# Performance work log

Measured on AMD Instinct MI355X. Metric: run time of the kernel, lower is better.

Reference implementation:

```python
import jax, jax.numpy as jnp
import numpy as np

N_NODES = 50000
N_EDGES = 800000
NUM_GRAPHS = 500
BN_EPS = 1e-5


def setup_inputs() -> dict:
    key = jax.random.key(0)
    ks = jax.random.split(key, 8)
    x = jax.random.normal(ks[0], (N_NODES, 33), dtype=jnp.float32)
    edge_index = jax.random.randint(ks[1], (2, N_EDGES), 0, N_NODES, dtype=jnp.int64)
    batch = jnp.sort(jax.random.randint(ks[2], (N_NODES,), 0, NUM_GRAPHS, dtype=jnp.int64))
    # Xavier-ish scaled weights
    W0 = jax.random.normal(ks[3], (33, 100), dtype=jnp.float32) * (2.0 / (33 + 100)) ** 0.5
    Wrest = jax.random.normal(ks[4], (3, 100, 100), dtype=jnp.float32) * (2.0 / 200) ** 0.5
    b = jnp.zeros((4, 100), dtype=jnp.float32)
    gamma = jnp.ones((4, 100), dtype=jnp.float32)
    beta = jnp.zeros((4, 100), dtype=jnp.float32)
    Wout = jax.random.normal(ks[5], (100, 200), dtype=jnp.float32) * (2.0 / 300) ** 0.5
    bout = jnp.zeros((200,), dtype=jnp.float32)
    return {"x": x, "edge_index": edge_index, "batch": batch, "W0": W0,
            "Wrest": Wrest, "b": b, "gamma": gamma, "beta": beta,
            "Wout": Wout, "bout": bout}


def reference(x, edge_index, batch, W0, Wrest, b, gamma, beta, Wout, bout):
    N = x.shape[0]
    # GCN normalization with self-loops (gcn_norm): shared across layers
    loops = jnp.arange(N, dtype=edge_index.dtype)
    src = jnp.concatenate([edge_index[0], loops])
    dst = jnp.concatenate([edge_index[1], loops])
    deg = jax.ops.segment_sum(jnp.ones_like(dst, dtype=x.dtype), dst, num_segments=N)
    dinv = jnp.where(deg > 0, jax.lax.rsqrt(deg), 0.0)
    norm = dinv[src] * dinv[dst]  # [E+N]

    Ws = [W0, Wrest[0], Wrest[1], Wrest[2]]
    h = x
    for layer in range(4):
        m = h @ Ws[layer]                                   # [N, out_c]
        agg = jax.ops.segment_sum(norm[:, None] * m[src], dst, num_segments=N)
        agg = agg + b[layer]
        # BatchNorm1d (batch statistics, biased variance)
        mean = agg.mean(axis=0)
        var = agg.var(axis=0)
        hbn = (agg - mean) * jax.lax.rsqrt(var + BN_EPS) * gamma[layer] + beta[layer]
        h = jax.nn.relu(hbn) if layer < 3 else hbn          # dropout is identity in eval

    g = jax.ops.segment_sum(h, batch, num_segments=NUM_GRAPHS)  # global_add_pool
    out = g @ Wout + bout
    return jnp.where(out > 0, out, 0.1 * out)  # LeakyReLU(0.1)
```

## Files before the change

### kernel.cpp

```cpp
#include <hip/hip_runtime.h>

#define NNODES 50000
#define NEDGES 800000
#define NGRAPH 500
#define CH 100
#define CIN0 33
#define BN_EPS 1e-5f
#define NSHARD 8
#define SHSTRIDE 1024
#define NBUK 196
#define BEPW 2048

#define SCAN_TPB 256
#define SCAN_IPT 4
#define SCAN_TILE (SCAN_TPB * SCAN_IPT)
#define SCAN_BLOCKS ((NNODES + SCAN_TILE - 1) / SCAN_TILE)

typedef __attribute__((ext_vector_type(8))) short short8;
typedef __attribute__((ext_vector_type(4))) float f32x4;

__device__ inline unsigned pack_bf16(float x, float y) {
    unsigned xb = __float_as_uint(x);
    unsigned yb = __float_as_uint(y);
    xb += 0x7FFF + ((xb >> 16) & 1);
    yb += 0x7FFF + ((yb >> 16) & 1);
    return (xb >> 16) | (yb & 0xFFFF0000u);
}
__device__ inline float unp_lo(unsigned v) { return __uint_as_float(v << 16); }
__device__ inline float unp_hi(unsigned v) { return __uint_as_float(v & 0xFFFF0000u); }

__global__ void k_prep(const float* __restrict__ x, unsigned* __restrict__ xb,
                       int* __restrict__ cnt, float* __restrict__ stats,
                       float* __restrict__ gbuf,
                       const float* __restrict__ Wrest, unsigned* __restrict__ whi,
                       unsigned* __restrict__ wlo,
                       const float* __restrict__ W0, unsigned* __restrict__ w0hi,
                       unsigned* __restrict__ w0lo,
                       unsigned* __restrict__ Z0, unsigned* __restrict__ Z1) {
    int i = blockIdx.x * blockDim.x + threadIdx.x;
    if (i < (NNODES + 1) * 17) {
        int r = i / 17, s = i - r * 17;
        if (r >= NNODES) xb[i] = 0u;
        else {
            float a = x[r * CIN0 + 2 * s];
            float b = (2 * s + 1 < CIN0) ? x[r * CIN0 + 2 * s + 1] : 0.f;
            xb[i] = pack_bf16(a, b);
        }
    }
    if (i < NNODES) { cnt[i] = 0; gbuf[i] = 0.f; }
    if (i < NSHARD * SHSTRIDE) stats[i] = 0.f;
    if (i < 3 * 112 * 64) {
        int l = i / 7168, rem = i % 7168;
        int c = rem >> 6, ku = rem & 63;
        int k0 = 2 * ku;
        float w0 = 0.f, w1 = 0.f;
        if (c < CH && k0 < CH) {
            w0 = Wrest[l * 10000 + k0 * CH + c];
            if (k0 + 1 < CH) w1 = Wrest[l * 10000 + (k0 + 1) * CH + c];
        }
        unsigned hh = pack_bf16(w0, w1);
        whi[i] = hh;
        wlo[i] = pack_bf16(w0 - unp_lo(hh), w1 - unp_hi(hh));
    }
    if (i < 112 * 32) {
        int c = i >> 5, ku = i & 31;
        int k0 = 2 * ku;
        float w0 = 0.f, w1 = 0.f;
        if (c < CH && k0 < CIN0) {
            w0 = W0[k0 * CH + c];
            if (k0 + 1 < CIN0) w1 = W0[(k0 + 1) * CH + c];
        }
        unsigned hh = pack_bf16(w0, w1);
        w0hi[i] = hh;
        w0lo[i] = pack_bf16(w0 - unp_lo(hh), w1 - unp_hi(hh));
    }
    if (i < 50) {
        Z0[(size_t)NNODES * 50 + i] = 0u;
        Z1[(size_t)NNODES * 50 + i] = 0u;
    }
}

__global__ void k_hist(const int* __restrict__ dst, int* __restrict__ cnt) {
    int e = blockIdx.x * blockDim.x + threadIdx.x;
    if (e < NEDGES) atomicAdd(&cnt[dst[e]], 1);
}

__global__ void k_scan1(const int* __restrict__ cnt, int* __restrict__ rowptr,
                        int* __restrict__ blkSums, float* __restrict__ dinv,
                        int* __restrict__ bcnt) {
    __shared__ int ts[SCAN_TPB];
    __shared__ int bsum[4];
    int tid = threadIdx.x;
    if (tid < 4) bsum[tid] = 0;
    int base = blockIdx.x * SCAN_TILE + tid * SCAN_IPT;
    int v[SCAN_IPT];
    int s = 0, cact = 0;
    #pragma unroll
    for (int j = 0; j < SCAN_IPT; ++j) {
        int i = base + j;
        int c = (i < NNODES) ? cnt[i] : 0;
        if (i < NNODES) dinv[i] = rsqrtf((float)(c + 1));
        v[j] = (c + 7) & ~7;
        s += v[j];
        cact += c;
    }
    ts[tid] = s;
    __syncthreads();
    atomicAdd(&bsum[(tid * SCAN_IPT) >> 8], cact);
    for (int off = 1; off < SCAN_TPB; off <<= 1) {
        int add = (tid >= off) ? ts[tid - off] : 0;
        __syncthreads();
        ts[tid] += add;
        __syncthreads();
    }
    int run = ts[tid] - s;
    #pragma unroll
    for (int j = 0; j < SCAN_IPT; ++j) {
        int i = base + j;
        if (i < NNODES) rowptr[i] = run;
        run += v[j];
    }
    if (tid == SCAN_TPB - 1) blkSums[blockIdx.x] = ts[tid];
    if (tid < 4) {
        int b = blockIdx.x * 4 + tid;
        if (b < NBUK) bcnt[b] = bsum[tid];
    }
}

__global__ void k_scan2b(const int* __restrict__ blkSums, int* __restrict__ blkOff,
                         int* __restrict__ rowptr, const int* __restrict__ bcnt,
                         int* __restrict__ bbase, int* __restrict__ gbkcur) {
    __shared__ int ts[256];
    int t = threadIdx.x;
    if (t == 0) {
        int run = 0;
        for (int i = 0; i < SCAN_BLOCKS; ++i) { blkOff[i] = run; run += blkSums[i]; }
        rowptr[NNODES] = run;
    }
    int v = (t < NBUK) ? bcnt[t] : 0;
    ts[t] = v;
    __syncthreads();
    for (int off = 1; off < 256; off <<= 1) {
        int a = (t >= off) ? ts[t - off] : 0;
        __syncthreads();
        ts[t] += a;
        __syncthreads();
    }
    int excl = ts[t] - v;
    if (t < NBUK) { bbase[t] = excl; gbkcur[t] = excl; }
    if (t == NBUK - 1) bbase[NBUK] = ts[t];
}

__global__ void k_scan3(int* __restrict__ rowptr, const int* __restrict__ blkOff) {
    int off = blkOff[blockIdx.x];
    int base = blockIdx.x * SCAN_TILE + threadIdx.x * SCAN_IPT;
    #pragma unroll
    for (int j = 0; j < SCAN_IPT; ++j) {
        int i = base + j;
        if (i < NNODES) rowptr[i] += off;
    }
}

__global__ __launch_bounds__(256) void k_bin(const int* __restrict__ src,
                                             const int* __restrict__ dst,
                                             const float* __restrict__ dinv,
                                             int* __restrict__ gbkcur,
                                             uint2* __restrict__ ebuf) {
    __shared__ int hist[256], ofs[256], lcnt[256], bbaseL[256];
    __shared__ int totS;
    __shared__ uint2 stage[BEPW];
    int tid = threadIdx.x;
    hist[tid] = 0; lcnt[tid] = 0;
    __syncthreads();
    int e0 = blockIdx.x * BEPW;
    unsigned sv[8]; int dv[8]; bool ok[8];
    #pragma unroll
    for (int j = 0; j < 8; ++j) {
        int e = e0 + j * 256 + tid;
        ok[j] = e < NEDGES;
        int s = ok[j] ? src[e] : 0;
        dv[j] = ok[j] ? dst[e] : 0;
        if (ok[j]) {
            unsigned db = __float_as_uint(dinv[s]);
            db += 0x7FFF + ((db >> 16) & 1);
            sv[j] = (unsigned)s | (db & 0xFFFF0000u);
            atomicAdd(&hist[dv[j] >> 8], 1);
        }
    }
    __syncthreads();
    int v = hist[tid];
    ofs[tid] = v;
    __syncthreads();
    for (int off = 1; off < 256; off <<= 1) {
        int a = (tid >= off) ? ofs[tid - off] : 0;
        __syncthreads();
        ofs[tid] += a;
        __syncthreads();
    }
    if (tid == 255) totS = ofs[255];
    int excl = ofs[tid] - v;
    __syncthreads();
    ofs[tid] = excl;
    if (tid < NBUK && v > 0) bbaseL[tid] = atomicAdd(&gbkcur[tid], v);
    __syncthreads();
    #pragma unroll
    for (int j = 0; j < 8; ++j) {
        if (ok[j]) {
            int b = dv[j] >> 8;
            int idx = atomicAdd(&lcnt[b], 1);
            stage[ofs[b] + idx] = make_uint2(sv[j], (unsigned)dv[j]);
        }
    }
    __syncthreads();
    int tot = totS;
    #pragma unroll
    for (int j = 0; j < 8; ++j) {
        int slot = j * 256 + tid;
        if (slot < tot) {
            uint2 p = stage[slot];
            int b = (int)(p.y >> 8);
            ebuf[bbaseL[b] + (slot - ofs[b])] = p;
        }
    }
}

__global__ __launch_bounds__(256) void k_place(const uint2* __restrict__ ebuf,
                                               const int* __restrict__ bbase,
                                               const int* __restrict__ rowptr,
                                               unsigned* __restrict__ ew) {
    __shared__ int lcur[256];
    int b = blockIdx.x, t = threadIdx.x;
    int lo = b * 256;
    int n = NNODES - lo; if (n > 256) n = 256;
    if (t < n) lcur[t] = rowptr[lo + t];
    __syncthreads();
    int e0 = bbase[b], e1 = bbase[b + 1];
    for (int e = e0 + t; e < e1; e += 256) {
        uint2 p = ebuf[e];
        int pos = atomicAdd(&lcur[p.y & 255], 1);
        ew[pos] = p.x;
    }
    __syncthreads();
    if (t < n) {
        int end = rowptr[lo + t + 1];
        for (int q = lcur[t]; q < end; ++q) ew[q] = NNODES;
    }
}

template<int CPACK, int RB, int KS, bool BN>
__global__ __launch_bounds__(512, 8) void k_fused(
    const unsigned* __restrict__ h, const unsigned* __restrict__ Whi,
    const unsigned* __restrict__ Wlo, const float* __restrict__ bias,
    const int* __restrict__ rowptr, const unsigned* __restrict__ ew,
    const float* __restrict__ dinv,
    const float* __restrict__ pgsum, const float* __restrict__ pgsq,
    const float* __restrict__ gamma, const float* __restrict__ beta,
    unsigned* __restrict__ Zout, float* __restrict__ gsum, float* __restrict__ gsq) {
    constexpr int RBY = KS * 64;
    __shared__ __align__(16) unsigned char aS[64 * RBY];
    __shared__ __align__(16) unsigned char wB[112 * 128];
    __shared__ float sSum[CH], sSq[CH];
    int tid = threadIdx.x;
    for (int i = tid; i < CH; i += 512) { sSum[i] = 0.f; sSq[i] = 0.f; }
    for (int idx = tid; idx < 112 * 8; idx += 512) {
        int c = idx >> 3, j = idx & 7;
        uint4 v = *(const uint4*)(Whi + c * (KS * 16) + j * 4);
        *(uint4*)(wB + ((unsigned)(c * 128 + j * 16) ^ ((c & 7) << 4))) = v;
    }
    int w = tid >> 6, lane = tid & 63;
    int row0 = blockIdx.x * 64;
    const char* __restrict__ hb = (const char*)h;
    bool act = lane < CPACK;
    unsigned l4 = (unsigned)(lane << 2);
    float scx = 0.f, shx = 0.f, scy = 0.f, shy = 0.f;
    if (BN && act) {
        float sx = 0.f, sy = 0.f, qx = 0.f, qy = 0.f;
        #pragma unroll
        for (int sh = 0; sh < NSHARD; ++sh) {
            float2 s2 = ((const float2*)(pgsum + sh * SHSTRIDE))[lane];
            float2 q2 = ((const float2*)(pgsq + sh * SHSTRIDE))[lane];
            sx += s2.x; sy += s2.y; qx += q2.x; qy += q2.y;
        }
        constexpr float invN = 1.f / NNODES;
        float2 g2 = ((const float2*)gamma)[lane];
        float2 b2 = ((const float2*)beta)[lane];
        float mx = sx * invN, my = sy * invN;
        float vx = qx * invN - mx * mx, vy = qy * invN - my * my;
        scx = g2.x * rsqrtf(vx + BN_EPS); shx = b2.x - mx * scx;
        scy = g2.y * rsqrtf(vy + BN_EPS); shy = b2.y - my * scy;
    }
    for (int ni = 0; ni < 8; ++ni) {
        int r = w * 8 + ni;
        int node = row0 + r;
        float ax = 0.f, ay = 0.f, di = 0.f;
        if (node < NNODES) {
            int p0 = __builtin_amdgcn_readfirstlane(rowptr[node]);
            int p1 = __builtin_amdgcn_readfirstlane(rowptr[node + 1]);
            di = dinv[node];
            if (act) {
                unsigned hv = h[(size_t)node * CPACK + lane];
                float fx = unp_lo(hv), fy = unp_hi(hv);
                if (BN) {
                    fx = fmaxf(fmaf(fx, scx, shx), 0.f);
                    fy = fmaxf(fmaf(fy, scy, shy), 0.f);
                }
                ax = di * fx; ay = di * fy;
            }
            const uint4* __restrict__ E4 = (const uint4*)(ew + p0);
            int n8 = (p1 - p0) >> 3;
            for (int q = 0; q < n8; ++q) {
                uint4 ea = E4[2 * q];
                uint4 eb = E4[2 * q + 1];
                unsigned ee[8] = {ea.x, ea.y, ea.z, ea.w, eb.x, eb.y, eb.z, eb.w};
                if (act) {
                    unsigned v[8];
                    #pragma unroll
                    for (int t = 0; t < 8; ++t)
                        v[t] = *(const unsigned*)(hb + (ee[t] & 0xFFFFu) * (unsigned)RB + l4);
                    #pragma unroll
                    for (int t = 0; t < 8; ++t) {
                        float vx = unp_lo(v[t]), vy = unp_hi(v[t]);
                        if (BN) {
                            vx = fmaxf(fmaf(vx, scx, shx), 0.f);
                            vy = fmaxf(fmaf(vy, scy, shy), 0.f);
                        }
                        float wgt = unp_hi(ee[t]);
                        ax = fmaf(wgt, vx, ax); ay = fmaf(wgt, vy, ay);
                    }
                }
            }
        }
        unsigned val = act ? pack_bf16(di * ax, di * ay) : 0u;
        if (lane < RBY / 4)
            *(unsigned*)(aS + ((unsigned)(r * RBY + lane * 4) ^ ((r & 7) << 4))) = val;
    }
    __syncthreads();
    int wm = w & 3, wh = w >> 2;
    int lr = lane & 15, lg = lane >> 4;
    f32x4 acc[4];
    #pragma unroll
    for (int nt = 0; nt < 4; ++nt) acc[nt] = (f32x4){0.f, 0.f, 0.f, 0.f};
    int ar = wm * 16 + lr;
    unsigned aswz = (unsigned)((ar & 7) << 4);
    #pragma unroll
    for (int ch = 0; ch < KS; ++ch) {
        if (ch) {
            __syncthreads();
            const unsigned* Wp = (ch >= KS / 2) ? Wlo : Whi;
            int p = (KS > 2) ? (ch & 1) : 0;
            for (int idx = tid; idx < 112 * 8; idx += 512) {
                int c = idx >> 3, j = idx & 7;
                uint4 v = *(const uint4*)(Wp + c * (KS * 16) + p * 32 + j * 4);
                *(uint4*)(wB + ((unsigned)(c * 128 + j * 16) ^ ((c & 7) << 4))) = v;
            }
            __syncthreads();
        }
        int p = (KS > 2) ? (ch & 1) : 0;
        #pragma unroll
        for (int ksl = 0; ksl < 2; ++ksl) {
            int ks = p * 2 + ksl;
            short8 af = *(const short8*)(aS + ((unsigned)(ar * RBY + ks * 64 + lg * 16) ^ aswz));
            #pragma unroll
            for (int nt = 0; nt < 4; ++nt) {
                if (wh && nt == 3) continue;
                int c = (wh * 4 + nt) * 16 + lr;
                short8 bb = *(const short8*)(wB + ((unsigned)(c * 128 + ksl * 64 + lg * 16) ^ ((c & 7) << 4)));
                acc[nt] = __builtin_amdgcn_mfma_f32_16x16x32_bf16(af, bb, acc[nt], 0, 0, 0);
            }
        }
    }
    #pragma unroll
    for (int nt = 0; nt < 4; ++nt) {
        if (wh && nt == 3) continue;
        int c = (wh * 4 + nt) * 16 + lr;
        bool cok = c < CH;
        float bcol = cok ? bias[c] : 0.f;
        float s = 0.f, q = 0.f;
        #pragma unroll
        for (int r = 0; r < 4; ++r) {
            int row = row0 + wm * 16 + lg * 4 + r;
            float z = acc[nt][r] + bcol;
            float zo = __shfl_xor(z, 1);
            if (cok && row < NNODES) {
                if ((lane & 1) == 0)
                    Zout[(size_t)row * 50 + (c >> 1)] = pack_bf16(z, zo);
                s += z; q += z * z;
            }
        }
        s += __shfl_xor(s, 16); s += __shfl_xor(s, 32);
        q += __shfl_xor(q, 16); q += __shfl_xor(q, 32);
        if (lane < 16 && cok) { atomicAdd(&sSum[c], s); atomicAdd(&sSq[c], q); }
    }
    __syncthreads();
    int sh = (blockIdx.x & (NSHARD - 1)) * SHSTRIDE;
    if (tid < CH) { atomicAdd(&gsum[sh + tid], sSum[tid]); atomicAdd(&gsq[sh + tid], sSq[tid]); }
}

__global__ void k_pool(const unsigned* __restrict__ Zl, const int* __restrict__ batch,
                       const float* __restrict__ gsum, const float* __restrict__ gsq,
                       const float* __restrict__ gamma, const float* __restrict__ beta,
                       float* __restrict__ g) {
    int gid = blockIdx.x;
    int part = blockIdx.y;
    int lo = 0, hi = NNODES;
    while (lo < hi) { int mid = (lo + hi) >> 1; if (batch[mid] < gid) lo = mid + 1; else hi = mid; }
    int start = lo;
    hi = NNODES;
    while (lo < hi) { int mid = (lo + hi) >> 1; if (batch[mid] < gid + 1) lo = mid + 1; else hi = mid; }
    int end = lo;
    int len = end - start;
    int cb = (len + 3) >> 2;
    int s = start + part * cb;
    int e = s + cb; if (e > end) e = end;
    if (s >= e) return;
    int t = threadIdx.x;
    if (t >= 50) return;
    float su = 0.f, sv = 0.f, qu = 0.f, qv = 0.f;
    #pragma unroll
    for (int sh = 0; sh < NSHARD; ++sh) {
        float2 s2 = ((const float2*)(gsum + sh * SHSTRIDE))[t];
        float2 q2 = ((const float2*)(gsq + sh * SHSTRIDE))[t];
        su += s2.x; sv += s2.y; qu += q2.x; qv += q2.y;
    }
    constexpr float invN = 1.f / NNODES;
    float2 g2 = ((const float2*)gamma)[t];
    float2 b2 = ((const float2*)beta)[t];
    float mx = su * invN, my = sv * invN;
    float vx = qu * invN - mx * mx, vy = qv * invN - my * my;
    float scx = g2.x * rsqrtf(vx + BN_EPS), shx = b2.x - mx * scx;
    float scy = g2.y * rsqrtf(vy + BN_EPS), shy = b2.y - my * scy;
    float sx = 0.f, sy = 0.f;
    for (int r = s; r < e; ++r) {
        unsigned v = Zl[(size_t)r * 50 + t];
        sx += unp_lo(v); sy += unp_hi(v);
    }
    float n = (float)(e - s);
    atomicAdd(&g[gid * CH + 2 * t], sx * scx + n * shx);
    atomicAdd(&g[gid * CH + 2 * t + 1], sy * scy + n * shy);
}

__global__ __launch_bounds__(256) void k_out(const float* __restrict__ g,
                                             const float* __restrict__ Wout,
                                             const float* __restrict__ bout,
                                             float* __restrict__ out) {
    __shared__ float gS[CH];
    int gid = blockIdx.x, tid = threadIdx.x;
    if (tid < CH) gS[tid] = g[gid * CH + tid];
    __syncthreads();
    if (tid >= 200) return;
    float acc = bout[tid];
    for (int k = 0; k < CH; ++k) acc += gS[k] * Wout[k * 200 + tid];
    out[gid * 200 + tid] = acc > 0.f ? acc : 0.1f * acc;
}

extern "C" void kernel_launch(void* const* d_in, const int* in_sizes, int n_in,
                              void* d_out, int out_size, void* d_ws, size_t ws_size,
                              hipStream_t stream) {
    const float* x = (const float*)d_in[0];
    const int* ei = (const int*)d_in[1];
    const int* batch = (const int*)d_in[2];
    const float* W0 = (const float*)d_in[3];
    const float* Wrest = (const float*)d_in[4];
    const float* b = (const float*)d_in[5];
    const float* gamma = (const float*)d_in[6];
    const float* beta = (const float*)d_in[7];
    const float* Wout = (const float*)d_in[8];
    const float* bout = (const float*)d_in[9];
    float* out = (float*)d_out;
    const int* srcA = ei;
    const int* dstA = ei + NEDGES;

    char* wsb = (char*)d_ws;
    size_t off = 0;
    auto alloc = [&](size_t elems) -> void* {
        void* p = (void*)(wsb + off);
        off += ((elems + 7) & ~(size_t)7) * 4;
        return p;
    };
    int* cnt = (int*)alloc(NNODES);
    int* rowptr = (int*)alloc(NNODES + 1);
    float* dinv = (float*)alloc(NNODES);
    int* scanBlk = (int*)alloc(64);
    int* scanOff = (int*)alloc(64);
    int* bcnt = (int*)alloc(256);
    int* bbase = (int*)alloc(256);
    int* gbkcur = (int*)alloc(256);
    float* stats = (float*)alloc(NSHARD * SHSTRIDE);
    unsigned* ew = (unsigned*)alloc((size_t)NEDGES + 8 * NNODES);
    uint2* ebuf = (uint2*)alloc(2 * (size_t)NEDGES);
    unsigned* xb = (unsigned*)alloc((size_t)(NNODES + 1) * 17);
    unsigned* wthi = (unsigned*)alloc(3 * 112 * 64);
    unsigned* wtlo = (unsigned*)alloc(3 * 112 * 64);
    unsigned* w0hi = (unsigned*)alloc(112 * 32);
    unsigned* w0lo = (unsigned*)alloc(112 * 32);
    unsigned* Z0 = (unsigned*)alloc((size_t)(NNODES + 1) * 50);
    unsigned* Z1 = (unsigned*)alloc((size_t)(NNODES + 1) * 50);
    float* gbuf = (float*)alloc((size_t)NGRAPH * CH);
    (void)ws_size; (void)n_in; (void)in_sizes; (void)out_size;

    hipLaunchKernelGGL(k_prep, dim3(((NNODES + 1) * 17 + 255) / 256), dim3(256), 0, stream,
                       x, xb, cnt, stats, gbuf, Wrest, wthi, wtlo, W0, w0hi, w0lo, Z0, Z1);
    hipLaunchKernelGGL(k_hist, dim3((NEDGES + 255) / 256), dim3(256), 0, stream, dstA, cnt);
    hipLaunchKernelGGL(k_scan1, dim3(SCAN_BLOCKS), dim3(SCAN_TPB), 0, stream,
                       cnt, rowptr, scanBlk, dinv, bcnt);
    hipLaunchKernelGGL(k_scan2b, dim3(1), dim3(256), 0, stream,
                       scanBlk, scanOff, rowptr, bcnt, bbase, gbkcur);
    hipLaunchKernelGGL(k_scan3, dim3(SCAN_BLOCKS), dim3(SCAN_TPB), 0, stream, rowptr, scanOff);
    hipLaunchKernelGGL(k_bin, dim3((NEDGES + BEPW - 1) / BEPW), dim3(256), 0, stream,
                       srcA, dstA, dinv, gbkcur, ebuf);
    hipLaunchKernelGGL(k_place, dim3(NBUK), dim3(256), 0, stream, ebuf, bbase, rowptr, ew);

    const int NTILE = (NNODES + 63) / 64;
    hipLaunchKernelGGL((k_fused<17, 68, 2, false>), dim3(NTILE), dim3(512), 0, stream,
                       xb, w0hi, w0lo, b, rowptr, ew, dinv,
                       (const float*)nullptr, (const float*)nullptr,
                       (const float*)nullptr, (const float*)nullptr,
                       Z0, stats + 0 * 128, stats + 512 + 0 * 128);
    unsigned* Zp[4] = {Z0, Z1, Z0, Z1};
    for (int l = 1; l < 4; ++l) {
        hipLaunchKernelGGL((k_fused<50, 200, 4, true>), dim3(NTILE), dim3(512), 0, stream,
                           Zp[l - 1], wthi + (l - 1) * 7168, wtlo + (l - 1) * 7168, b + l * CH,
                           rowptr, ew, dinv,
                           stats + (l - 1) * 128, stats + 512 + (l - 1) * 128,
                           gamma + (l - 1) * CH, beta + (l - 1) * CH,
                           Zp[l], stats + l * 128, stats + 512 + l * 128);
    }
    hipLaunchKernelGGL(k_pool, dim3(NGRAPH, 4), dim3(64), 0, stream, Z1, batch,
                       stats + 3 * 128, stats + 512 + 3 * 128, gamma + 3 * CH, beta + 3 * CH, gbuf);
    hipLaunchKernelGGL(k_out, dim3(NGRAPH), dim3(256), 0, stream, gbuf, Wout, bout, out);
}
```

Baseline: 333.3 us.

## Fold block-offset scan fixup into k_place and prefetch next weight chunk during MFMA

Drops the k_scan3 kernel. k_place now adds the per-block scan offset itself while loading row pointers, and writes the final row pointers to a new rp2 array that the fused layers read. Inside the fused GEMM, the next weight chunk is loaded from global into registers before the current chunk's MFMAs, then written to shared memory afterwards. This is meant to hide global load latency behind compute and save one kernel launch, at the cost of extra registers for the prefetch buffers.

Measured after the change: 326.0 us. -2.2%, faster.

```diff
diff --git a/kernel.cpp b/kernel.cpp
--- a/kernel.cpp
+++ b/kernel.cpp
@@ -128,14 +128,14 @@
 }
 
 __global__ void k_scan2b(const int* __restrict__ blkSums, int* __restrict__ blkOff,
-                         int* __restrict__ rowptr, const int* __restrict__ bcnt,
+                         int* __restrict__ rp2, const int* __restrict__ bcnt,
                          int* __restrict__ bbase, int* __restrict__ gbkcur) {
     __shared__ int ts[256];
     int t = threadIdx.x;
     if (t == 0) {
         int run = 0;
         for (int i = 0; i < SCAN_BLOCKS; ++i) { blkOff[i] = run; run += blkSums[i]; }
-        rowptr[NNODES] = run;
+        rp2[NNODES] = run;
     }
     int v = (t < NBUK) ? bcnt[t] : 0;
     ts[t] = v;
@@ -149,16 +149,6 @@
     int excl = ts[t] - v;
     if (t < NBUK) { bbase[t] = excl; gbkcur[t] = excl; }
     if (t == NBUK - 1) bbase[NBUK] = ts[t];
-}
-
-__global__ void k_scan3(int* __restrict__ rowptr, const int* __restrict__ blkOff) {
-    int off = blkOff[blockIdx.x];
-    int base = blockIdx.x * SCAN_TILE + threadIdx.x * SCAN_IPT;
-    #pragma unroll
-    for (int j = 0; j < SCAN_IPT; ++j) {
-        int i = base + j;
-        if (i < NNODES) rowptr[i] += off;
-    }
 }
 
 __global__ __launch_bounds__(256) void k_bin(const int* __restrict__ src,
@@ -227,12 +217,19 @@
 __global__ __launch_bounds__(256) void k_place(const uint2* __restrict__ ebuf,
                                                const int* __restrict__ bbase,
                                                const int* __restrict__ rowptr,
+                                               const int* __restrict__ blkOff,
+                                               int* __restrict__ rp2,
                                                unsigned* __restrict__ ew) {
     __shared__ int lcur[256];
     int b = blockIdx.x, t = threadIdx.x;
     int lo = b * 256;
     int n = NNODES - lo; if (n > 256) n = 256;
-    if (t < n) lcur[t] = rowptr[lo + t];
+    if (t < n) {
+        int node = lo + t;
+        int base = rowptr[node] + blkOff[node >> 10];
+        lcur[t] = base;
+        rp2[node] = base;
+    }
     __syncthreads();
     int e0 = bbase[b], e1 = bbase[b + 1];
     for (int e = e0 + t; e < e1; e += 256) {
@@ -242,7 +239,8 @@
     }
     __syncthreads();
     if (t < n) {
-        int end = rowptr[lo + t + 1];
+        int idx = lo + t + 1;
+        int end = (idx < NNODES) ? (rowptr[idx] + blkOff[idx >> 10]) : rp2[NNODES];
         for (int q = lcur[t]; q < end; ++q) ew[q] = NNODES;
     }
 }
@@ -342,18 +340,21 @@
     for (int nt = 0; nt < 4; ++nt) acc[nt] = (f32x4){0.f, 0.f, 0.f, 0.f};
     int ar = wm * 16 + lr;
     unsigned aswz = (unsigned)((ar & 7) << 4);
+    uint4 pv0, pv1;
     #pragma unroll
     for (int ch = 0; ch < KS; ++ch) {
-        if (ch) {
-            __syncthreads();
-            const unsigned* Wp = (ch >= KS / 2) ? Wlo : Whi;
-            int p = (KS > 2) ? (ch & 1) : 0;
-            for (int idx = tid; idx < 112 * 8; idx += 512) {
+        if (ch + 1 < KS) {
+            const unsigned* Wp = (ch + 1 >= KS / 2) ? Wlo : Whi;
+            int pn = (KS > 2) ? ((ch + 1) & 1) : 0;
+            {
+                int c = tid >> 3, j = tid & 7;
+                pv0 = *(const uint4*)(Wp + c * (KS * 16) + pn * 32 + j * 4);
+            }
+            if (tid < 384) {
+                int idx = tid + 512;
                 int c = idx >> 3, j = idx & 7;
-                uint4 v = *(const uint4*)(Wp + c * (KS * 16) + p * 32 + j * 4);
-                *(uint4*)(wB + ((unsigned)(c * 128 + j * 16) ^ ((c & 7) << 4))) = v;
-            }
-            __syncthreads();
+                pv1 = *(const uint4*)(Wp + c * (KS * 16) + pn * 32 + j * 4);
+            }
         }
         int p = (KS > 2) ? (ch & 1) : 0;
         #pragma unroll
@@ -367,6 +368,19 @@
                 short8 bb = *(const short8*)(wB + ((unsigned)(c * 128 + ksl * 64 + lg * 16) ^ ((c & 7) << 4)));
                 acc[nt] = __builtin_amdgcn_mfma_f32_16x16x32_bf16(af, bb, acc[nt], 0, 0, 0);
             }
+        }
+        if (ch + 1 < KS) {
+            __syncthreads();
+            {
+                int c = tid >> 3, j = tid & 7;
+                *(uint4*)(wB + ((unsigned)(c * 128 + j * 16) ^ ((c & 7) << 4))) = pv0;
+            }
+            if (tid < 384) {
+                int idx = tid + 512;
+                int c = idx >> 3, j = idx & 7;
+                *(uint4*)(wB + ((unsigned)(c * 128 + j * 16) ^ ((c & 7) << 4))) = pv1;
+            }
+            __syncthreads();
         }
     }
     #pragma unroll
@@ -479,6 +493,7 @@
     };
     int* cnt = (int*)alloc(NNODES);
     int* rowptr = (int*)alloc(NNODES + 1);
+    int* rp2 = (int*)alloc(NNODES + 1);
     float* dinv = (float*)alloc(NNODES);
     int* scanBlk = (int*)alloc(64);
     int* scanOff = (int*)alloc(64);
@@ -504,15 +519,15 @@
     hipLaunchKernelGGL(k_scan1, dim3(SCAN_BLOCKS), dim3(SCAN_TPB), 0, stream,
                        cnt, rowptr, scanBlk, dinv, bcnt);
     hipLaunchKernelGGL(k_scan2b, dim3(1), dim3(256), 0, stream,
-                       scanBlk, scanOff, rowptr, bcnt, bbase, gbkcur);
-    hipLaunchKernelGGL(k_scan3, dim3(SCAN_BLOCKS), dim3(SCAN_TPB), 0, stream, rowptr, scanOff);
+                       scanBlk, scanOff, rp2, bcnt, bbase, gbkcur);
     hipLaunchKernelGGL(k_bin, dim3((NEDGES + BEPW - 1) / BEPW), dim3(256), 0, stream,
                        srcA, dstA, dinv, gbkcur, ebuf);
-    hipLaunchKernelGGL(k_place, dim3(NBUK), dim3(256), 0, stream, ebuf, bbase, rowptr, ew);
+    hipLaunchKernelGGL(k_place, dim3(NBUK), dim3(256), 0, stream,
+                       ebuf, bbase, rowptr, scanOff, rp2, ew);
 
     const int NTILE = (NNODES + 63) / 64;
     hipLaunchKernelGGL((k_fused<17, 68, 2, false>), dim3(NTILE), dim3(512), 0, stream,
-                       xb, w0hi, w0lo, b, rowptr, ew, dinv,
+                       xb, w0hi, w0lo, b, rp2, ew, dinv,
                        (const float*)nullptr, (const float*)nullptr,
                        (const float*)nullptr, (const float*)nullptr,
                        Z0, stats + 0 * 128, stats + 512 + 0 * 128);
@@ -520,7 +535,7 @@
     for (int l = 1; l < 4; ++l) {
         hipLaunchKernelGGL((k_fused<50, 200, 4, true>), dim3(NTILE), dim3(512), 0, stream,
                            Zp[l - 1], wthi + (l - 1) * 7168, wtlo + (l - 1) * 7168, b + l * CH,
-                           rowptr, ew, dinv,
+                           rp2, ew, dinv,
                            stats + (l - 1) * 128, stats + 512 + (l - 1) * 128,
                            gamma + (l - 1) * CH, beta + (l - 1) * CH,
                            Zp[l], stats + l * 128, stats + 512 + l * 128);
```
